# Performance work log

Measured on AMD Instinct MI355X. Metric: run time of the kernel, lower is better.

## Reference

```python
import jax, jax.numpy as jnp
import numpy as np

LN_EPS = 1e-5
L2_EPS = 1e-6
TAU = 0.07

def _proj(x, W, b, g, be):
    # Linear + LayerNorm (dropout is identity in eval)
    y = x @ W.T + b
    mu = jnp.mean(y, axis=-1, keepdims=True)
    var = jnp.var(y, axis=-1, keepdims=True)
    return (y - mu) * jax.lax.rsqrt(var + LN_EPS) * g + be

def _l2norm(x):
    return x / (jnp.linalg.norm(x, axis=-1, keepdims=True) + L2_EPS)

def setup_inputs() -> dict:
    key = jax.random.key(0)
    ks = iter(jax.random.split(key, 16))
    B, C, D = 2048, 512, 256
    dims = {"text": 1024, "image": 1024, "audio": 512, "tab": 256}
    inp = {}
    for n, d in dims.items():
        inp[f"f_{n}"] = jax.random.normal(next(ks), (B, d), jnp.float32)
        inp[f"W_{n}"] = jax.random.normal(next(ks), (D, d), jnp.float32) * (1.0 / np.sqrt(d))
        inp[f"b_{n}"] = jnp.zeros((D,), jnp.float32)
        inp[f"g_{n}"] = jnp.ones((D,), jnp.float32)
        inp[f"be_{n}"] = jnp.zeros((D,), jnp.float32)
    inp["U"] = jax.random.normal(next(ks), (C, D), jnp.float32) * (1.0 / np.sqrt(D))
    inp["O"] = jax.random.normal(next(ks), (C, D), jnp.float32) * (1.0 / np.sqrt(D))
    inp["cls_bias"] = jnp.zeros((C,), jnp.float32)
    return inp

def reference(f_text, f_image, f_audio, f_tab,
              W_text, b_text, g_text, be_text,
              W_image, b_image, g_image, be_image,
              W_audio, b_audio, g_audio, be_audio,
              W_tab, b_tab, g_tab, be_tab,
              U, O, cls_bias):
    # Per-modality projection -> Z: [B, M, D]
    Z = jnp.stack([
        _proj(f_text, W_text, b_text, g_text, be_text),
        _proj(f_image, W_image, b_image, g_image, be_image),
        _proj(f_audio, W_audio, b_audio, g_audio, be_audio),
        _proj(f_tab, W_tab, b_tab, g_tab, be_tab),
    ], axis=1)
    Zn = _l2norm(Z)            # [B, M, D]
    Un = _l2norm(U)            # [C, D]
    sim = jnp.einsum('bmd,cd->bmc', Zn, Un) / max(TAU, 1e-6)
    r = jax.nn.softmax(sim, axis=1)                 # softmax over modalities M
    Cmix = jnp.einsum('bmc,bmd->bcd', r, Z)         # [B, C, D]
    logits = jnp.einsum('cd,bcd->bc', O, Cmix) + cls_bias
    OjZi = jnp.einsum('cd,bmd->bmc', O, Z)
    contrib = OjZi * r
    return logits, r, sim, contrib
```

## Files before the change

kernel.cpp:

```cpp
#include <hip/hip_runtime.h>
#include <math.h>

typedef __attribute__((ext_vector_type(8))) short short8;
typedef __attribute__((ext_vector_type(4))) float f32x4;
typedef unsigned short u16;

constexpr int Bn = 2048, Mn = 4, Cn = 512, Dn = 256;
constexpr size_t LOGITS_OFF = 0;
constexpr size_t R_OFF   = (size_t)Bn * Cn;
constexpr size_t SIM_OFF = R_OFF + (size_t)Bn * Mn * Cn;
constexpr size_t CTR_OFF = SIM_OFF + (size_t)Bn * Mn * Cn;
constexpr float INV_TAU = 1.0f / 0.07f;

#define WAIT_STEADY asm volatile("s_waitcnt vmcnt(5) lgkmcnt(0)" ::: "memory")
#define WAIT_LAST   asm volatile("s_waitcnt vmcnt(0) lgkmcnt(0)" ::: "memory")

__device__ __forceinline__ unsigned short f2bf(float f) {
  unsigned u = __float_as_uint(f);
  u += 0x7fffu + ((u >> 16) & 1u);
  return (unsigned short)(u >> 16);
}

__device__ __forceinline__ void gload16(const void* g, void* l) {
  __builtin_amdgcn_global_load_lds(
      (const __attribute__((address_space(1))) void*)g,
      (__attribute__((address_space(3))) void*)l, 16, 0, 0);
}

struct CvtArgs {
  const float* src[6];
  u16* dst[6];
};

__global__ __launch_bounds__(256) void cvt_kernel(CvtArgs a,
                                                  const float* __restrict__ U,
                                                  float* __restrict__ invU) {
  const int blk = blockIdx.x;
  if (blk >= 480) {
    int c = (blk - 480) * 4 + (threadIdx.x >> 6);
    int lane = threadIdx.x & 63;
    float4 v = *(const float4*)&U[(size_t)c * Dn + lane * 4];
    float s = v.x*v.x + v.y*v.y + v.z*v.z + v.w*v.w;
    #pragma unroll
    for (int m = 32; m >= 1; m >>= 1) s += __shfl_xor(s, m, 64);
    if (lane == 0) invU[c] = 1.0f / (sqrtf(s) + 1e-6f);
    return;
  }
  int c = blk * 256 + threadIdx.x;
  const int ends[6] = {32768, 65536, 81920, 90112, 106496, 122880};
  int ai = 0, base = 0;
  #pragma unroll
  for (int i = 0; i < 5; i++)
    if (c >= ends[i]) { ai = i + 1; base = ends[i]; }
  int idx = (c - base) * 8;
  const float4* s = (const float4*)(a.src[ai] + idx);
  float4 v0 = s[0], v1 = s[1];
  uint4 p;
  p.x = f2bf(v0.x) | ((unsigned)f2bf(v0.y) << 16);
  p.y = f2bf(v0.z) | ((unsigned)f2bf(v0.w) << 16);
  p.z = f2bf(v1.x) | ((unsigned)f2bf(v1.y) << 16);
  p.w = f2bf(v1.z) | ((unsigned)f2bf(v1.w) << 16);
  *(uint4*)(a.dst[ai] + idx) = p;
}

struct ProjArgs {
  const float* f[4];
  const float* b[4];
  const float* g[4];
  const float* be[4];
  const u16* Wb[4];
  int K[4];
};

__global__ __launch_bounds__(256, 2) void proj_kernel(ProjArgs a,
                                                      u16* __restrict__ Zb,
                                                      float* __restrict__ invZ) {
  const int m = blockIdx.y;
  const int K = a.K[m];
  const int NS = K >> 5;
  const float* __restrict__ F = a.f[m];
  const u16* __restrict__ Wm = a.Wb[m];

  const int tid = threadIdx.x;
  const int w = tid >> 6, l = tid & 63;
  const int rg = l >> 4, c16 = l & 15;
  const int row0 = blockIdx.x * 16;

  __shared__ u16 aS[3][512];
  __shared__ u16 bS[3][8192];
  __shared__ float pS[4][16][2];
  __shared__ float qS[4][16];
  __shared__ u16 zS[16][264];

  const int arow = tid >> 4;
  const int akk  = (tid & 15) * 2;
  const float* asrc = F + (size_t)(row0 + arow) * K + akk;
  const int awi = ((akk >> 3) * 16 + arow) * 8 + (akk & 7);

  f32x4 acc[4];
  #pragma unroll
  for (int i = 0; i < 4; i++) acc[i] = (f32x4){0.f, 0.f, 0.f, 0.f};

  auto bstage = [&](int nb, int k0) {
    #pragma unroll
    for (int ii = 0; ii < 4; ii++)
      gload16(Wm + (size_t)(w * 64 + l) * K + k0 + ii * 8,
              &bS[nb][(ii * 256 + w * 64) * 8]);
  };
  auto aload = [&](int t) -> float2 {
    return *(const float2*)(asrc + ((size_t)t << 5));
  };
  auto awrite = [&](int nb, float2 v) {
    unsigned p = f2bf(v.x) | ((unsigned)f2bf(v.y) << 16);
    *(unsigned*)&aS[nb][awi] = p;
  };
  auto compute = [&](int cb) {
    short8 av = *(const short8*)&aS[cb][(rg * 16 + c16) * 8];
    #pragma unroll
    for (int nf = 0; nf < 4; nf++) {
      short8 bv = *(const short8*)&bS[cb][(rg * 256 + w * 64 + nf * 16 + c16) * 8];
      acc[nf] = __builtin_amdgcn_mfma_f32_16x16x32_bf16(av, bv, acc[nf], 0, 0, 0);
    }
  };

  float2 aA = aload(0);
  bstage(0, 0);
  float2 aB = aload(1);
  bstage(1, 32);
  awrite(0, aA);

  for (int tt = 0; tt < NS; tt += 2) {
    WAIT_STEADY;
    __builtin_amdgcn_s_barrier();
    if (tt + 2 < NS) { aA = aload(tt + 2); bstage((tt + 2) % 3, (tt + 2) << 5); }
    awrite((tt + 1) % 3, aB);
    compute(tt % 3);
    if (tt < NS - 2) WAIT_STEADY; else WAIT_LAST;
    __builtin_amdgcn_s_barrier();
    if (tt + 3 < NS) { aB = aload(tt + 3); bstage((tt + 3) % 3, (tt + 3) << 5); }
    if (tt + 2 < NS) awrite((tt + 2) % 3, aA);
    compute((tt + 1) % 3);
  }

  float bb[4], gg[4], ee[4];
  #pragma unroll
  for (int nf = 0; nf < 4; nf++) {
    int col = w * 64 + nf * 16 + c16;
    bb[nf] = a.b[m][col];
    gg[nf] = a.g[m][col];
    ee[nf] = a.be[m][col];
  }
  float s[4] = {0,0,0,0}, s2[4] = {0,0,0,0};
  #pragma unroll
  for (int nf = 0; nf < 4; nf++)
    #pragma unroll
    for (int j = 0; j < 4; j++) {
      float y = acc[nf][j] + bb[nf];
      acc[nf][j] = y;
      s[j] += y; s2[j] += y * y;
    }
  #pragma unroll
  for (int msk = 8; msk >= 1; msk >>= 1)
    #pragma unroll
    for (int j = 0; j < 4; j++) {
      s[j]  += __shfl_xor(s[j],  msk, 64);
      s2[j] += __shfl_xor(s2[j], msk, 64);
    }
  if (c16 == 0)
    #pragma unroll
    for (int j = 0; j < 4; j++) {
      pS[w][rg*4+j][0] = s[j];
      pS[w][rg*4+j][1] = s2[j];
    }
  __syncthreads();
  float mu[4], rs[4];
  #pragma unroll
  for (int j = 0; j < 4; j++) {
    int row = rg*4 + j;
    float st  = pS[0][row][0] + pS[1][row][0] + pS[2][row][0] + pS[3][row][0];
    float s2t = pS[0][row][1] + pS[1][row][1] + pS[2][row][1] + pS[3][row][1];
    mu[j] = st * (1.0f/256.0f);
    float var = s2t * (1.0f/256.0f) - mu[j]*mu[j];
    rs[j] = rsqrtf(var + 1e-5f);
  }
  float zs[4] = {0,0,0,0};
  #pragma unroll
  for (int nf = 0; nf < 4; nf++)
    #pragma unroll
    for (int j = 0; j < 4; j++) {
      float z = (acc[nf][j] - mu[j]) * rs[j] * gg[nf] + ee[nf];
      acc[nf][j] = z;
      zs[j] += z * z;
    }
  #pragma unroll
  for (int msk = 8; msk >= 1; msk >>= 1)
    #pragma unroll
    for (int j = 0; j < 4; j++) zs[j] += __shfl_xor(zs[j], msk, 64);
  if (c16 == 0)
    #pragma unroll
    for (int j = 0; j < 4; j++) qS[w][rg*4+j] = zs[j];
  __syncthreads();
  #pragma unroll
  for (int j = 0; j < 4; j++) {
    int row = rg*4 + j;
    float zt = qS[0][row] + qS[1][row] + qS[2][row] + qS[3][row];
    float inv = 1.0f / (sqrtf(zt) + 1e-6f);
    if (c16 == 0 && w == 0)
      invZ[(size_t)(row0 + row) * 4 + m] = inv;
  }
  #pragma unroll
  for (int nf = 0; nf < 4; nf++)
    #pragma unroll
    for (int j = 0; j < 4; j++)
      zS[rg*4 + j][w*64 + nf*16 + c16] = f2bf(acc[nf][j]);
  __syncthreads();
  #pragma unroll
  for (int i = 0; i < 2; i++) {
    int c = tid + i * 256;
    int row = c >> 5, colc = (c & 31) * 8;
    uint4 v = *(const uint4*)&zS[row][colc];
    *(uint4*)(Zb + ((size_t)(row0 + row) * 4 + m) * 256 + colc) = v;
  }
}

__global__ __launch_bounds__(256, 2) void dual_kernel(
    const u16* __restrict__ Zb,
    const u16* __restrict__ Ub,
    const u16* __restrict__ Ob,
    const float* __restrict__ invZ, const float* __restrict__ invU,
    const float* __restrict__ cls_bias, float* __restrict__ out) {
  const int tid = threadIdx.x;
  const int w = tid >> 6, l = tid & 63;
  const int wr = w >> 1, wc2 = w & 1;
  const int rg = l >> 4, c16 = l & 15;
  const int row0 = blockIdx.x * 64;
  const int col0 = blockIdx.y * 128;

  __shared__ u16 aS[3][2048];
  __shared__ u16 uS[3][4096];
  __shared__ u16 oS[3][4096];

  f32x4 accU[2][4], accO[2][4];
  #pragma unroll
  for (int i = 0; i < 2; i++)
    #pragma unroll
    for (int j = 0; j < 4; j++) {
      accU[i][j] = (f32x4){0.f, 0.f, 0.f, 0.f};
      accO[i][j] = (f32x4){0.f, 0.f, 0.f, 0.f};
    }

  auto stage = [&](int nb, int k0) {
    gload16(Zb + (size_t)(row0 + l) * 256 + k0 + w * 8, &aS[nb][w * 512]);
    #pragma unroll
    for (int jj = 0; jj < 2; jj++) {
      gload16(Ub + (size_t)(col0 + jj * 64 + l) * 256 + k0 + w * 8,
              &uS[nb][(w * 128 + jj * 64) * 8]);
      gload16(Ob + (size_t)(col0 + jj * 64 + l) * 256 + k0 + w * 8,
              &oS[nb][(w * 128 + jj * 64) * 8]);
    }
  };
  auto compute = [&](int cb) {
    short8 av0 = *(const short8*)&aS[cb][(rg * 64 + wr * 32 + c16) * 8];
    short8 av1 = *(const short8*)&aS[cb][(rg * 64 + wr * 32 + 16 + c16) * 8];
    #pragma unroll
    for (int nf = 0; nf < 4; nf++) {
      int chunk = rg * 128 + wc2 * 64 + nf * 16 + c16;
      short8 uv = *(const short8*)&uS[cb][chunk * 8];
      accU[0][nf] = __builtin_amdgcn_mfma_f32_16x16x32_bf16(av0, uv, accU[0][nf], 0, 0, 0);
      accU[1][nf] = __builtin_amdgcn_mfma_f32_16x16x32_bf16(av1, uv, accU[1][nf], 0, 0, 0);
      short8 ov = *(const short8*)&oS[cb][chunk * 8];
      accO[0][nf] = __builtin_amdgcn_mfma_f32_16x16x32_bf16(av0, ov, accO[0][nf], 0, 0, 0);
      accO[1][nf] = __builtin_amdgcn_mfma_f32_16x16x32_bf16(av1, ov, accO[1][nf], 0, 0, 0);
    }
  };

  stage(0, 0);
  stage(1, 32);
  #pragma unroll
  for (int t = 0; t < 8; t++) {
    if (t < 7) WAIT_STEADY; else WAIT_LAST;
    __builtin_amdgcn_s_barrier();
    if (t + 2 < 8) stage((t + 2) % 3, (t + 2) << 5);
    compute(t % 3);
  }

  #pragma unroll
  for (int mf = 0; mf < 2; mf++) {
    const int bmb = row0 + wr * 32 + mf * 16 + rg * 4;
    const f32x4 iz = *(const f32x4*)&invZ[bmb];
    const int bidx = bmb >> 2;
    #pragma unroll
    for (int nf = 0; nf < 4; nf++) {
      int col = col0 + wc2 * 64 + nf * 16 + c16;
      float iu = invU[col] * INV_TAU;
      f32x4 sU = accU[mf][nf], sO = accO[mf][nf];
      float sim0 = sU[0] * iz[0] * iu;
      float sim1 = sU[1] * iz[1] * iu;
      float sim2 = sU[2] * iz[2] * iu;
      float sim3 = sU[3] * iz[3] * iu;
      float mx = fmaxf(fmaxf(sim0, sim1), fmaxf(sim2, sim3));
      float e0 = __expf(sim0 - mx), e1 = __expf(sim1 - mx);
      float e2 = __expf(sim2 - mx), e3 = __expf(sim3 - mx);
      float rinv = 1.0f / (e0 + e1 + e2 + e3);
      float r0 = e0 * rinv, r1 = e1 * rinv, r2 = e2 * rinv, r3 = e3 * rinv;
      float ct0 = sO[0] * r0, ct1 = sO[1] * r1, ct2 = sO[2] * r2, ct3 = sO[3] * r3;
      size_t sb = (size_t)bmb * Cn + col;
      out[SIM_OFF + sb]        = sim0;
      out[SIM_OFF + sb + Cn]   = sim1;
      out[SIM_OFF + sb + 2*Cn] = sim2;
      out[SIM_OFF + sb + 3*Cn] = sim3;
      out[R_OFF + sb]          = r0;
      out[R_OFF + sb + Cn]     = r1;
      out[R_OFF + sb + 2*Cn]   = r2;
      out[R_OFF + sb + 3*Cn]   = r3;
      out[CTR_OFF + sb]        = ct0;
      out[CTR_OFF + sb + Cn]   = ct1;
      out[CTR_OFF + sb + 2*Cn] = ct2;
      out[CTR_OFF + sb + 3*Cn] = ct3;
      out[LOGITS_OFF + (size_t)bidx * Cn + col] =
          ct0 + ct1 + ct2 + ct3 + cls_bias[col];
    }
  }
}

extern "C" void kernel_launch(void* const* d_in, const int* in_sizes, int n_in,
                              void* d_out, int out_size, void* d_ws, size_t ws_size,
                              hipStream_t stream) {
  const int fi[4] = {0, 5, 10, 15};
  const int Ks[4] = {1024, 1024, 512, 256};

  char* ws = (char*)d_ws;
  u16* Zb  = (u16*)(ws + 0);
  u16* Wb0 = (u16*)(ws + 4194304);
  u16* Wb1 = (u16*)(ws + 4718592);
  u16* Wb2 = (u16*)(ws + 5242880);
  u16* Wb3 = (u16*)(ws + 5505024);
  u16* Ub  = (u16*)(ws + 5636096);
  u16* Ob  = (u16*)(ws + 5898240);
  float* invZ = (float*)(ws + 6160384);
  float* invU = (float*)(ws + 6193152);
  u16* Wb[4] = {Wb0, Wb1, Wb2, Wb3};

  ProjArgs pa;
  for (int m = 0; m < 4; m++) {
    pa.f[m]  = (const float*)d_in[fi[m] + 0];
    pa.b[m]  = (const float*)d_in[fi[m] + 2];
    pa.g[m]  = (const float*)d_in[fi[m] + 3];
    pa.be[m] = (const float*)d_in[fi[m] + 4];
    pa.Wb[m] = Wb[m];
    pa.K[m]  = Ks[m];
  }
  const float* U        = (const float*)d_in[20];
  const float* O        = (const float*)d_in[21];
  const float* cls_bias = (const float*)d_in[22];

  CvtArgs ca;
  ca.src[0] = (const float*)d_in[1];   ca.dst[0] = Wb0;
  ca.src[1] = (const float*)d_in[6];   ca.dst[1] = Wb1;
  ca.src[2] = (const float*)d_in[11];  ca.dst[2] = Wb2;
  ca.src[3] = (const float*)d_in[16];  ca.dst[3] = Wb3;
  ca.src[4] = U;                       ca.dst[4] = Ub;
  ca.src[5] = O;                       ca.dst[5] = Ob;

  float* out = (float*)d_out;

  cvt_kernel<<<608, 256, 0, stream>>>(ca, U, invU);
  proj_kernel<<<dim3(Bn / 16, 4), 256, 0, stream>>>(pa, Zb, invZ);
  dual_kernel<<<dim3((Bn * Mn) / 64, Cn / 128), 256, 0, stream>>>(
      Zb, Ub, Ob, invZ, invU, cls_bias, out);
}
```

Baseline: 180.1 us.

## Stage full A tile in LDS and stream weights directly from global in both GEMMs

The projection kernel now uses 512 threads. It converts the whole 16-row activation tile to bf16 into LDS up front, then has each wave load W fragments straight from global memory, with no triple-buffered LDS pipeline or barriers. The dual kernel loads the full 64x256 Z tile into LDS once, shrinks the column tile to 64, and reads U/O fragments directly from global (cached), doubling the grid. The aim is to remove per-step barrier and waitcnt overhead and raise occupancy. The trade-off is no load/compute overlap within a block and uncoalesced 16-byte global reads for the B operands, which now rely on L2/L1 reuse.

```diff
diff --git a/kernel.cpp b/kernel.cpp
--- a/kernel.cpp
+++ b/kernel.cpp
@@ -11,9 +11,6 @@
 constexpr size_t SIM_OFF = R_OFF + (size_t)Bn * Mn * Cn;
 constexpr size_t CTR_OFF = SIM_OFF + (size_t)Bn * Mn * Cn;
 constexpr float INV_TAU = 1.0f / 0.07f;
-
-#define WAIT_STEADY asm volatile("s_waitcnt vmcnt(5) lgkmcnt(0)" ::: "memory")
-#define WAIT_LAST   asm volatile("s_waitcnt vmcnt(0) lgkmcnt(0)" ::: "memory")
 
 __device__ __forceinline__ unsigned short f2bf(float f) {
   unsigned u = __float_as_uint(f);
@@ -72,7 +69,7 @@
   int K[4];
 };
 
-__global__ __launch_bounds__(256, 2) void proj_kernel(ProjArgs a,
+__global__ __launch_bounds__(512, 4) void proj_kernel(ProjArgs a,
                                                       u16* __restrict__ Zb,
                                                       float* __restrict__ invZ) {
   const int m = blockIdx.y;
@@ -86,73 +83,54 @@
   const int rg = l >> 4, c16 = l & 15;
   const int row0 = blockIdx.x * 16;
 
-  __shared__ u16 aS[3][512];
-  __shared__ u16 bS[3][8192];
-  __shared__ float pS[4][16][2];
-  __shared__ float qS[4][16];
+  __shared__ u16 aS[16 * 1024];
+  __shared__ float pS[8][16][2];
+  __shared__ float qS[8][16];
   __shared__ u16 zS[16][264];
 
-  const int arow = tid >> 4;
-  const int akk  = (tid & 15) * 2;
-  const float* asrc = F + (size_t)(row0 + arow) * K + akk;
-  const int awi = ((akk >> 3) * 16 + arow) * 8 + (akk & 7);
-
-  f32x4 acc[4];
-  #pragma unroll
-  for (int i = 0; i < 4; i++) acc[i] = (f32x4){0.f, 0.f, 0.f, 0.f};
-
-  auto bstage = [&](int nb, int k0) {
-    #pragma unroll
-    for (int ii = 0; ii < 4; ii++)
-      gload16(Wm + (size_t)(w * 64 + l) * K + k0 + ii * 8,
-              &bS[nb][(ii * 256 + w * 64) * 8]);
-  };
-  auto aload = [&](int t) -> float2 {
-    return *(const float2*)(asrc + ((size_t)t << 5));
-  };
-  auto awrite = [&](int nb, float2 v) {
-    unsigned p = f2bf(v.x) | ((unsigned)f2bf(v.y) << 16);
-    *(unsigned*)&aS[nb][awi] = p;
-  };
-  auto compute = [&](int cb) {
-    short8 av = *(const short8*)&aS[cb][(rg * 16 + c16) * 8];
-    #pragma unroll
-    for (int nf = 0; nf < 4; nf++) {
-      short8 bv = *(const short8*)&bS[cb][(rg * 256 + w * 64 + nf * 16 + c16) * 8];
-      acc[nf] = __builtin_amdgcn_mfma_f32_16x16x32_bf16(av, bv, acc[nf], 0, 0, 0);
-    }
-  };
-
-  float2 aA = aload(0);
-  bstage(0, 0);
-  float2 aB = aload(1);
-  bstage(1, 32);
-  awrite(0, aA);
-
-  for (int tt = 0; tt < NS; tt += 2) {
-    WAIT_STEADY;
-    __builtin_amdgcn_s_barrier();
-    if (tt + 2 < NS) { aA = aload(tt + 2); bstage((tt + 2) % 3, (tt + 2) << 5); }
-    awrite((tt + 1) % 3, aB);
-    compute(tt % 3);
-    if (tt < NS - 2) WAIT_STEADY; else WAIT_LAST;
-    __builtin_amdgcn_s_barrier();
-    if (tt + 3 < NS) { aB = aload(tt + 3); bstage((tt + 3) % 3, (tt + 3) << 5); }
-    if (tt + 2 < NS) awrite((tt + 2) % 3, aA);
-    compute((tt + 1) % 3);
-  }
-
-  float bb[4], gg[4], ee[4];
-  #pragma unroll
-  for (int nf = 0; nf < 4; nf++) {
-    int col = w * 64 + nf * 16 + c16;
+  const int niter = (K * 16) >> 12;
+  for (int it = 0; it < niter; it++) {
+    int i = it * 512 + tid;
+    int row = i & 15, kc = i >> 4;
+    const float* src = F + (size_t)(row0 + row) * K + kc * 8;
+    float4 v0 = *(const float4*)src;
+    float4 v1 = *(const float4*)(src + 4);
+    short8 p;
+    p[0] = (short)f2bf(v0.x); p[1] = (short)f2bf(v0.y);
+    p[2] = (short)f2bf(v0.z); p[3] = (short)f2bf(v0.w);
+    p[4] = (short)f2bf(v1.x); p[5] = (short)f2bf(v1.y);
+    p[6] = (short)f2bf(v1.z); p[7] = (short)f2bf(v1.w);
+    *(short8*)&aS[i * 8] = p;
+  }
+  __syncthreads();
+
+  f32x4 acc[2];
+  acc[0] = (f32x4){0.f, 0.f, 0.f, 0.f};
+  acc[1] = (f32x4){0.f, 0.f, 0.f, 0.f};
+  const u16* b0p = Wm + (size_t)(w * 32 + c16) * K + rg * 8;
+  const u16* b1p = b0p + (size_t)16 * K;
+  const int abase = (rg * 16 + c16) * 8;
+
+  #pragma unroll 4
+  for (int t = 0; t < NS; t++) {
+    short8 av = *(const short8*)&aS[abase + t * 512];
+    short8 b0 = *(const short8*)(b0p + t * 32);
+    short8 b1 = *(const short8*)(b1p + t * 32);
+    acc[0] = __builtin_amdgcn_mfma_f32_16x16x32_bf16(av, b0, acc[0], 0, 0, 0);
+    acc[1] = __builtin_amdgcn_mfma_f32_16x16x32_bf16(av, b1, acc[1], 0, 0, 0);
+  }
+
+  float bb[2], gg[2], ee[2];
+  #pragma unroll
+  for (int nf = 0; nf < 2; nf++) {
+    int col = w * 32 + nf * 16 + c16;
     bb[nf] = a.b[m][col];
     gg[nf] = a.g[m][col];
     ee[nf] = a.be[m][col];
   }
   float s[4] = {0,0,0,0}, s2[4] = {0,0,0,0};
   #pragma unroll
-  for (int nf = 0; nf < 4; nf++)
+  for (int nf = 0; nf < 2; nf++)
     #pragma unroll
     for (int j = 0; j < 4; j++) {
       float y = acc[nf][j] + bb[nf];
@@ -177,15 +155,16 @@
   #pragma unroll
   for (int j = 0; j < 4; j++) {
     int row = rg*4 + j;
-    float st  = pS[0][row][0] + pS[1][row][0] + pS[2][row][0] + pS[3][row][0];
-    float s2t = pS[0][row][1] + pS[1][row][1] + pS[2][row][1] + pS[3][row][1];
+    float st = 0.f, s2t = 0.f;
+    #pragma unroll
+    for (int ww = 0; ww < 8; ww++) { st += pS[ww][row][0]; s2t += pS[ww][row][1]; }
     mu[j] = st * (1.0f/256.0f);
     float var = s2t * (1.0f/256.0f) - mu[j]*mu[j];
     rs[j] = rsqrtf(var + 1e-5f);
   }
   float zs[4] = {0,0,0,0};
   #pragma unroll
-  for (int nf = 0; nf < 4; nf++)
+  for (int nf = 0; nf < 2; nf++)
     #pragma unroll
     for (int j = 0; j < 4; j++) {
       float z = (acc[nf][j] - mu[j]) * rs[j] * gg[nf] + ee[nf];
@@ -203,27 +182,27 @@
   #pragma unroll
   for (int j = 0; j < 4; j++) {
     int row = rg*4 + j;
-    float zt = qS[0][row] + qS[1][row] + qS[2][row] + qS[3][row];
+    float zt = 0.f;
+    #pragma unroll
+    for (int ww = 0; ww < 8; ww++) zt += qS[ww][row];
     float inv = 1.0f / (sqrtf(zt) + 1e-6f);
     if (c16 == 0 && w == 0)
       invZ[(size_t)(row0 + row) * 4 + m] = inv;
   }
   #pragma unroll
-  for (int nf = 0; nf < 4; nf++)
+  for (int nf = 0; nf < 2; nf++)
     #pragma unroll
     for (int j = 0; j < 4; j++)
-      zS[rg*4 + j][w*64 + nf*16 + c16] = f2bf(acc[nf][j]);
-  __syncthreads();
-  #pragma unroll
-  for (int i = 0; i < 2; i++) {
-    int c = tid + i * 256;
-    int row = c >> 5, colc = (c & 31) * 8;
+      zS[rg*4 + j][w*32 + nf*16 + c16] = f2bf(acc[nf][j]);
+  __syncthreads();
+  {
+    int row = tid >> 5, colc = (tid & 31) * 8;
     uint4 v = *(const uint4*)&zS[row][colc];
     *(uint4*)(Zb + ((size_t)(row0 + row) * 4 + m) * 256 + colc) = v;
   }
 }
 
-__global__ __launch_bounds__(256, 2) void dual_kernel(
+__global__ __launch_bounds__(256, 4) void dual_kernel(
     const u16* __restrict__ Zb,
     const u16* __restrict__ Ub,
     const u16* __restrict__ Ob,
@@ -231,57 +210,51 @@
     const float* __restrict__ cls_bias, float* __restrict__ out) {
   const int tid = threadIdx.x;
   const int w = tid >> 6, l = tid & 63;
-  const int wr = w >> 1, wc2 = w & 1;
+  const int wr = w & 1, wc = w >> 1;
   const int rg = l >> 4, c16 = l & 15;
   const int row0 = blockIdx.x * 64;
-  const int col0 = blockIdx.y * 128;
-
-  __shared__ u16 aS[3][2048];
-  __shared__ u16 uS[3][4096];
-  __shared__ u16 oS[3][4096];
-
-  f32x4 accU[2][4], accO[2][4];
+  const int col0 = blockIdx.y * 64 + wc * 32;
+
+  __shared__ u16 aS[64 * 256];
+
+  #pragma unroll
+  for (int it = 0; it < 8; it++) {
+    int i = it * 256 + tid;
+    gload16(Zb + (size_t)(row0 + (i & 63)) * 256 + (i >> 6) * 8, &aS[i * 8]);
+  }
+  __syncthreads();
+
+  f32x4 accU[2][2], accO[2][2];
   #pragma unroll
   for (int i = 0; i < 2; i++)
     #pragma unroll
-    for (int j = 0; j < 4; j++) {
+    for (int j = 0; j < 2; j++) {
       accU[i][j] = (f32x4){0.f, 0.f, 0.f, 0.f};
       accO[i][j] = (f32x4){0.f, 0.f, 0.f, 0.f};
     }
-
-  auto stage = [&](int nb, int k0) {
-    gload16(Zb + (size_t)(row0 + l) * 256 + k0 + w * 8, &aS[nb][w * 512]);
-    #pragma unroll
-    for (int jj = 0; jj < 2; jj++) {
-      gload16(Ub + (size_t)(col0 + jj * 64 + l) * 256 + k0 + w * 8,
-              &uS[nb][(w * 128 + jj * 64) * 8]);
-      gload16(Ob + (size_t)(col0 + jj * 64 + l) * 256 + k0 + w * 8,
-              &oS[nb][(w * 128 + jj * 64) * 8]);
-    }
-  };
-  auto compute = [&](int cb) {
-    short8 av0 = *(const short8*)&aS[cb][(rg * 64 + wr * 32 + c16) * 8];
-    short8 av1 = *(const short8*)&aS[cb][(rg * 64 + wr * 32 + 16 + c16) * 8];
-    #pragma unroll
-    for (int nf = 0; nf < 4; nf++) {
-      int chunk = rg * 128 + wc2 * 64 + nf * 16 + c16;
-      short8 uv = *(const short8*)&uS[cb][chunk * 8];
-      accU[0][nf] = __builtin_amdgcn_mfma_f32_16x16x32_bf16(av0, uv, accU[0][nf], 0, 0, 0);
-      accU[1][nf] = __builtin_amdgcn_mfma_f32_16x16x32_bf16(av1, uv, accU[1][nf], 0, 0, 0);
-      short8 ov = *(const short8*)&oS[cb][chunk * 8];
-      accO[0][nf] = __builtin_amdgcn_mfma_f32_16x16x32_bf16(av0, ov, accO[0][nf], 0, 0, 0);
-      accO[1][nf] = __builtin_amdgcn_mfma_f32_16x16x32_bf16(av1, ov, accO[1][nf], 0, 0, 0);
-    }
-  };
-
-  stage(0, 0);
-  stage(1, 32);
-  #pragma unroll
+  const u16* u0p = Ub + (size_t)(col0 + c16) * 256 + rg * 8;
+  const u16* u1p = u0p + 16 * 256;
+  const u16* o0p = Ob + (size_t)(col0 + c16) * 256 + rg * 8;
+  const u16* o1p = o0p + 16 * 256;
+  const int ab0 = (rg * 64 + wr * 32 + c16) * 8;
+  const int ab1 = ab0 + 16 * 8;
+
+  #pragma unroll 4
   for (int t = 0; t < 8; t++) {
-    if (t < 7) WAIT_STEADY; else WAIT_LAST;
-    __builtin_amdgcn_s_barrier();
-    if (t + 2 < 8) stage((t + 2) % 3, (t + 2) << 5);
-    compute(t % 3);
+    short8 a0 = *(const short8*)&aS[ab0 + t * 2048];
+    short8 a1 = *(const short8*)&aS[ab1 + t * 2048];
+    short8 u0 = *(const short8*)(u0p + t * 32);
+    short8 u1 = *(const short8*)(u1p + t * 32);
+    short8 o0 = *(const short8*)(o0p + t * 32);
+    short8 o1 = *(const short8*)(o1p + t * 32);
+    accU[0][0] = __builtin_amdgcn_mfma_f32_16x16x32_bf16(a0, u0, accU[0][0], 0, 0, 0);
+    accU[0][1] = __builtin_amdgcn_mfma_f32_16x16x32_bf16(a0, u1, accU[0][1], 0, 0, 0);
+    accU[1][0] = __builtin_amdgcn_mfma_f32_16x16x32_bf16(a1, u0, accU[1][0], 0, 0, 0);
+    accU[1][1] = __builtin_amdgcn_mfma_f32_16x16x32_bf16(a1, u1, accU[1][1], 0, 0, 0);
+    accO[0][0] = __builtin_amdgcn_mfma_f32_16x16x32_bf16(a0, o0, accO[0][0], 0, 0, 0);
+    accO[0][1] = __builtin_amdgcn_mfma_f32_16x16x32_bf16(a0, o1, accO[0][1], 0, 0, 0);
+    accO[1][0] = __builtin_amdgcn_mfma_f32_16x16x32_bf16(a1, o0, accO[1][0], 0, 0, 0);
+    accO[1][1] = __builtin_amdgcn_mfma_f32_16x16x32_bf16(a1, o1, accO[1][1], 0, 0, 0);
   }
 
   #pragma unroll
@@ -290,8 +263,8 @@
     const f32x4 iz = *(const f32x4*)&invZ[bmb];
     const int bidx = bmb >> 2;
     #pragma unroll
-    for (int nf = 0; nf < 4; nf++) {
-      int col = col0 + wc2 * 64 + nf * 16 + c16;
+    for (int nf = 0; nf < 2; nf++) {
+      int col = col0 + nf * 16 + c16;
       float iu = invU[col] * INV_TAU;
       f32x4 sU = accU[mf][nf], sO = accO[mf][nf];
       float sim0 = sU[0] * iz[0] * iu;
@@ -365,7 +338,7 @@
   float* out = (float*)d_out;
 
   cvt_kernel<<<608, 256, 0, stream>>>(ca, U, invU);
-  proj_kernel<<<dim3(Bn / 16, 4), 256, 0, stream>>>(pa, Zb, invZ);
-  dual_kernel<<<dim3((Bn * Mn) / 64, Cn / 128), 256, 0, stream>>>(
+  proj_kernel<<<dim3(Bn / 16, 4), 512, 0, stream>>>(pa, Zb, invZ);
+  dual_kernel<<<dim3((Bn * Mn) / 64, Cn / 64), 256, 0, stream>>>(
       Zb, Ub, Ob, invZ, invU, cls_bias, out);
 }
```

New measurement: 171.4 us. 1.05x faster.
